# Kernel tuning notes

Measured on AMD Instinct MI355X. Metric: run time of the kernel, lower is better.

## Reference

```python
import jax, jax.numpy as jnp
import numpy as np

M, B, N, C, H = 3, 8, 512, 512, 8
HD = C // H
W_SCALE = 0.02  # keep attention logits in a sane range


def setup_inputs() -> dict:
    key = jax.random.key(0)
    ks = jax.random.split(key, 10)
    f32 = jnp.float32
    return {
        "x": jax.random.normal(ks[0], (M, B, N, C), f32),
        "Wq": jax.random.normal(ks[1], (M, C, C), f32) * W_SCALE,
        "bq": jax.random.normal(ks[2], (M, C), f32) * W_SCALE,
        "Wk": jax.random.normal(ks[3], (M, C, C), f32) * W_SCALE,
        "bk": jax.random.normal(ks[4], (M, C), f32) * W_SCALE,
        "Wv": jax.random.normal(ks[5], (M, C, C), f32) * W_SCALE,
        "bv": jax.random.normal(ks[6], (M, C), f32) * W_SCALE,
        "mw": jnp.ones((M, M), f32),
        "Wp": jax.random.normal(ks[7], (C, C), f32) * W_SCALE,
        "bp": jax.random.normal(ks[8], (C,), f32) * W_SCALE,
    }


def reference(x, Wq, bq, Wk, bk, Wv, bv, mw, Wp, bp):
    # x: [M,B,N,C] stacked modality features
    m, b, n, c = x.shape
    h, hd = H, c // H
    scale = hd ** -0.5

    def project(W, bias):
        y = jnp.einsum('mbnc,mcd->mbnd', x, W) + bias[:, None, None, :]
        return y.reshape(m, b, n, h, hd).transpose(0, 1, 3, 2, 4)  # [M,B,H,N,hd]

    q = project(Wq, bq)
    k = project(Wk, bk)
    v = project(Wv, bv)

    # all M*M pairwise attentions: i = query modality, j = key/value modality
    scores = jnp.einsum('ibhnd,jbhkd->ijbhnk', q, k) * scale  # [M,M,B,H,N,N]
    probs = jax.nn.softmax(scores, axis=-1)
    out = jnp.einsum('ijbhnk,jbhkd->ijbhnd', probs, v)
    out = out * mw[:, :, None, None, None, None]  # per-pair modal weight

    # sum over key-modality j, then mean over query-modality i
    fused = out.sum(axis=1).mean(axis=0)  # [B,H,N,hd]
    fused = fused.transpose(0, 2, 1, 3).reshape(b, n, c)  # [B,N,C]

    return jnp.einsum('bnc,cd->bnd', fused, Wp) + bp
```

## Files before the change

### kernel.cpp

```cpp
#include <hip/hip_runtime.h>
#include <stdint.h>

#define M_ 3
#define B_ 8
#define N_ 512
#define C_ 512
#define H_ 8
#define HD_ 64

typedef __bf16 bf16x8 __attribute__((ext_vector_type(8)));
typedef float f32x4 __attribute__((ext_vector_type(4)));
typedef float f32x16 __attribute__((ext_vector_type(16)));
typedef unsigned int u32x4 __attribute__((ext_vector_type(4)));

static __device__ __forceinline__ unsigned short f2bf(float f) {
  unsigned int u = __float_as_uint(f);
  unsigned int r = (u + 0x7FFFu + ((u >> 16) & 1u)) >> 16;
  return (unsigned short)r;
}
static __device__ __forceinline__ float bf2f(unsigned short s) {
  return __uint_as_float(((unsigned int)s) << 16);
}

static __device__ __forceinline__ void gll16(const void* g, void* l) {
  __builtin_amdgcn_global_load_lds(
      (const __attribute__((address_space(1))) unsigned int*)g,
      (__attribute__((address_space(3))) unsigned int*)l, 16, 0, 0);
}

__global__ void convert_x_kernel(const float* __restrict__ x,
                                 unsigned short* __restrict__ xb, int n4) {
  int i = blockIdx.x * 256 + threadIdx.x;
  if (i < n4) {
    float4 v = ((const float4*)x)[i];
    ushort4 o;
    o.x = f2bf(v.x); o.y = f2bf(v.y); o.z = f2bf(v.z); o.w = f2bf(v.w);
    ((ushort4*)xb)[i] = o;
  }
}

__global__ void transpose_w_kernel(const float* __restrict__ Wq, const float* __restrict__ Wk,
                                   const float* __restrict__ Wv, const float* __restrict__ Wp,
                                   unsigned short* __restrict__ Wqt, unsigned short* __restrict__ Wkt,
                                   unsigned short* __restrict__ Wvt, unsigned short* __restrict__ Wpt) {
  int z = blockIdx.z;
  const float* src; unsigned short* dst;
  if (z < 3)      { src = Wq + z * 262144;      dst = Wqt + z * 262144; }
  else if (z < 6) { src = Wk + (z - 3) * 262144; dst = Wkt + (z - 3) * 262144; }
  else if (z < 9) { src = Wv + (z - 6) * 262144; dst = Wvt + (z - 6) * 262144; }
  else            { src = Wp;                    dst = Wpt; }
  __shared__ unsigned short t[64][68];
  int r0 = blockIdx.x * 64, c0 = blockIdx.y * 64;
  int tr = threadIdx.x >> 4, tc = (threadIdx.x & 15) * 4;
#pragma unroll
  for (int it = 0; it < 4; ++it) {
    int r = tr + it * 16;
    float4 v = *(const float4*)&src[(size_t)(r0 + r) * 512 + c0 + tc];
    t[tc + 0][r] = f2bf(v.x); t[tc + 1][r] = f2bf(v.y);
    t[tc + 2][r] = f2bf(v.z); t[tc + 3][r] = f2bf(v.w);
  }
  __syncthreads();
#pragma unroll
  for (int it = 0; it < 4; ++it) {
    int d = tr + it * 16;
    ushort4 o;
    o.x = t[d][tc + 0]; o.y = t[d][tc + 1]; o.z = t[d][tc + 2]; o.w = t[d][tc + 3];
    *(ushort4*)&dst[(size_t)(c0 + d) * 512 + r0 + tc] = o;
  }
}

template <int MODE>
__launch_bounds__(256, 2)
__global__ void gemm128_kernel(const unsigned short* __restrict__ Aall,
                               const unsigned short* __restrict__ Bt0,
                               const unsigned short* __restrict__ Bt1,
                               const unsigned short* __restrict__ Bt2,
                               const float* __restrict__ bias0,
                               const float* __restrict__ bias1,
                               const float* __restrict__ bias2,
                               unsigned short* __restrict__ outQ,
                               unsigned short* __restrict__ outK,
                               unsigned short* __restrict__ outVt,
                               float* __restrict__ outF) {
  const int tid = threadIdx.x;
  const int wv = tid >> 6, l = tid & 63;
  const int wr = wv >> 1, wc = wv & 1;
  const int bm = blockIdx.x, bn = blockIdx.y;
  int m = 0, p = 0;
  const unsigned short* A; const unsigned short* Bt; const float* bias;
  if (MODE == 0) {
    int z = blockIdx.z; m = z / 3; p = z % 3;
    A = Aall + (size_t)m * (B_ * N_ * C_);
    Bt = (p == 0 ? Bt0 : p == 1 ? Bt1 : Bt2) + (size_t)m * (C_ * C_);
    bias = (p == 0 ? bias0 : p == 1 ? bias1 : bias2) + m * C_;
  } else {
    A = Aall; Bt = Bt0; bias = bias0;
  }
  __shared__ __align__(16) unsigned short lA[2][128 * 64];
  __shared__ __align__(16) unsigned short lB[2][128 * 64];
  f32x4 acc[4][4] = {};

  auto stage = [&](int buf, int kt) {
    int k0 = kt * 64;
#pragma unroll
    for (int it = 0; it < 4; ++it) {
      int f = (it * 256 + tid) * 16;
      int r = f >> 7, o = f & 127;
      int so = o ^ ((r & 7) << 4);
      gll16((const char*)A + ((size_t)(bm * 128 + r) * 512 + k0) * 2 + so,
            (char*)&lA[buf][0] + (it * 256 + wv * 64) * 16);
      gll16((const char*)Bt + ((size_t)(bn * 128 + r) * 512 + k0) * 2 + so,
            (char*)&lB[buf][0] + (it * 256 + wv * 64) * 16);
    }
  };

  stage(0, 0);
  __syncthreads();
  int buf = 0;
  for (int kt = 0; kt < 8; ++kt) {
    if (kt < 7) stage(buf ^ 1, kt + 1);
    bf16x8 aF[4][2], bF[4][2];
#pragma unroll
    for (int rt = 0; rt < 4; ++rt)
#pragma unroll
      for (int kf = 0; kf < 2; ++kf) {
        int rowA = wr * 64 + rt * 16 + (l & 15);
        int rowB = wc * 64 + rt * 16 + (l & 15);
        int kb = kf * 64 + (l >> 4) * 16;
        aF[rt][kf] = *(const bf16x8*)((const char*)&lA[buf][0] + rowA * 128 + (kb ^ ((rowA & 7) << 4)));
        bF[rt][kf] = *(const bf16x8*)((const char*)&lB[buf][0] + rowB * 128 + (kb ^ ((rowB & 7) << 4)));
      }
#pragma unroll
    for (int kf = 0; kf < 2; ++kf)
#pragma unroll
      for (int rt = 0; rt < 4; ++rt)
#pragma unroll
        for (int ct = 0; ct < 4; ++ct)
          acc[rt][ct] = __builtin_amdgcn_mfma_f32_16x16x32_bf16(aF[rt][kf], bF[ct][kf], acc[rt][ct], 0, 0, 0);
    __syncthreads();
    buf ^= 1;
  }

#pragma unroll
  for (int rt = 0; rt < 4; ++rt) {
    int rbase = bm * 128 + wr * 64 + rt * 16 + (l >> 4) * 4;
#pragma unroll
    for (int ct = 0; ct < 4; ++ct) {
      int col = bn * 128 + wc * 64 + ct * 16 + (l & 15);
      float bb = bias[col];
      if (MODE == 0) {
        int h = col >> 6, hd = col & 63;
        if (p < 2) {
          unsigned short* out = (p == 0 ? outQ : outK) + (size_t)m * (B_ * H_ * N_ * HD_);
#pragma unroll
          for (int jr = 0; jr < 4; ++jr) {
            int row = rbase + jr; int b = row >> 9, n = row & 511;
            out[(((size_t)(b * H_ + h) * N_ + n) * HD_) + hd] = f2bf(acc[rt][ct][jr] + bb);
          }
        } else {
          unsigned short* out = outVt + (size_t)m * (B_ * H_ * HD_ * N_);
          int row = rbase; int b = row >> 9, n = row & 511;
          ushort4 o;
          o.x = f2bf(acc[rt][ct][0] + bb);
          o.y = f2bf(acc[rt][ct][1] + bb);
          o.z = f2bf(acc[rt][ct][2] + bb);
          o.w = f2bf(acc[rt][ct][3] + bb);
          *(ushort4*)&out[(((size_t)(b * H_ + h) * HD_ + hd) * N_) + n] = o;
        }
      } else {
#pragma unroll
        for (int jr = 0; jr < 4; ++jr) {
          int row = rbase + jr;
          outF[(size_t)row * C_ + col] = acc[rt][ct][jr] + bb;
        }
      }
    }
  }
}

__launch_bounds__(256, 3)
__global__ void attn_kernel(const unsigned short* __restrict__ qg,
                            const unsigned short* __restrict__ kg,
                            const unsigned short* __restrict__ vg,
                            const float* __restrict__ mw,
                            unsigned short* __restrict__ att) {
  const int tid = threadIdx.x;
  const int wv = tid >> 6, l = tid & 63;
  const int hi = l >> 5, lq = l & 31;
  const int xcd = blockIdx.x & 7, slot = blockIdx.x >> 3;
  const int bh = (xcd << 3) | (slot & 7);
  const int qi = slot >> 3;
  const int qt = qi & 3, i = qi >> 2;
  const int b = bh >> 3, h = bh & 7;
  const int n0 = qt * 128;

  __shared__ __align__(16) unsigned short lK[2][64 * 64];
  __shared__ __align__(16) unsigned short lV[2][64 * 64];

  bf16x8 qB[4];
  {
    const unsigned short* qb = qg + (size_t)((i * B_ + b) * H_ + h) * N_ * HD_;
    int n = n0 + wv * 32 + lq;
#pragma unroll
    for (int ks = 0; ks < 4; ++ks)
      qB[ks] = *(const bf16x8*)&qb[(size_t)n * HD_ + ks * 16 + hi * 8];
  }

  f32x16 facc[2] = {};
  const float scale = 0.125f;

  for (int j = 0; j < 3; ++j) {
    const char* kb = (const char*)(kg + (size_t)((j * B_ + b) * H_ + h) * N_ * HD_);
    const char* vb = (const char*)(vg + (size_t)((j * B_ + b) * H_ + h) * HD_ * N_);
    auto stage = [&](int buf, int kt) {
#pragma unroll
      for (int it = 0; it < 2; ++it) {
        int f = (it * 256 + tid) * 16;
        int r = f >> 7, o = f & 127;
        int so = o ^ ((r & 7) << 4);
        gll16(kb + kt * 8192 + (f & ~127) + so, (char*)&lK[buf][0] + (it * 256 + wv * 64) * 16);
        gll16(vb + r * 1024 + kt * 128 + so,    (char*)&lV[buf][0] + (it * 256 + wv * 64) * 16);
      }
    };
    stage(0, 0);
    __syncthreads();
    f32x16 oacc[2] = {};
    float dAcc = 0.0f;
    int buf = 0;
    for (int kt = 0; kt < 8; ++kt) {
      if (kt < 7) stage(buf ^ 1, kt + 1);
#pragma unroll
      for (int kt2 = 0; kt2 < 2; ++kt2) {
        f32x16 sT = {};
#pragma unroll
        for (int ks = 0; ks < 4; ++ks) {
          int row = kt2 * 32 + lq;
          int col = (ks * 32 + hi * 16) ^ ((row & 7) << 4);
          bf16x8 kA = *(const bf16x8*)((const char*)&lK[buf][0] + row * 128 + col);
          sT = __builtin_amdgcn_mfma_f32_32x32x16_bf16(kA, qB[ks], sT, 0, 0, 0);
        }
        unsigned int c[8];
#pragma unroll
        for (int w = 0; w < 8; ++w) {
          float pa = __expf(sT[2 * w] * scale);
          float pb = __expf(sT[2 * w + 1] * scale);
          dAcc += pa + pb;
          c[w] = (unsigned int)f2bf(pa) | ((unsigned int)f2bf(pb) << 16);
        }
#pragma unroll
        for (int hs = 0; hs < 2; ++hs) {
          int ks = kt2 * 2 + hs;
          unsigned int p0 = (unsigned int)__shfl_xor((int)c[4 * hs + 0], 32, 64);
          unsigned int p1 = (unsigned int)__shfl_xor((int)c[4 * hs + 1], 32, 64);
          unsigned int p2 = (unsigned int)__shfl_xor((int)c[4 * hs + 2], 32, 64);
          unsigned int p3 = (unsigned int)__shfl_xor((int)c[4 * hs + 3], 32, 64);
          u32x4 pw;
          pw.x = hi ? p2 : c[4 * hs + 0];
          pw.y = hi ? p3 : c[4 * hs + 1];
          pw.z = hi ? c[4 * hs + 2] : p0;
          pw.w = hi ? c[4 * hs + 3] : p1;
          bf16x8 pA = __builtin_bit_cast(bf16x8, pw);
#pragma unroll
          for (int ht = 0; ht < 2; ++ht) {
            int row = ht * 32 + lq;
            int col = (ks * 32 + hi * 16) ^ ((row & 7) << 4);
            bf16x8 vB = *(const bf16x8*)((const char*)&lV[buf][0] + row * 128 + col);
            oacc[ht] = __builtin_amdgcn_mfma_f32_32x32x16_bf16(pA, vB, oacc[ht], 0, 0, 0);
          }
        }
      }
      __syncthreads();
      buf ^= 1;
    }
    float den = dAcc + __shfl_xor(dAcc, 32, 64);
    float t = mw[i * 3 + j] * (1.0f / 3.0f) / den;
#pragma unroll
    for (int reg = 0; reg < 16; ++reg) {
      int kkq = (reg & 3) + 8 * (reg >> 2) + 4 * hi;
      float tr = __shfl(t, kkq, 64);
      facc[0][reg] += oacc[0][reg] * tr;
      facc[1][reg] += oacc[1][reg] * tr;
    }
  }
  unsigned short* outp = att + (size_t)i * (B_ * N_ * C_);
#pragma unroll
  for (int ht = 0; ht < 2; ++ht)
#pragma unroll
    for (int reg = 0; reg < 16; ++reg) {
      int n = n0 + wv * 32 + (reg & 3) + 8 * (reg >> 2) + 4 * hi;
      int cc = h * 64 + ht * 32 + lq;
      outp[((size_t)b * N_ + n) * C_ + cc] = f2bf(facc[ht][reg]);
    }
}

__global__ void sum3_kernel(const unsigned short* __restrict__ a0,
                            const unsigned short* __restrict__ a1,
                            const unsigned short* __restrict__ a2,
                            unsigned short* __restrict__ o, int n4) {
  int idx = blockIdx.x * 256 + threadIdx.x;
  if (idx < n4) {
    ushort4 x0 = ((const ushort4*)a0)[idx];
    ushort4 x1 = ((const ushort4*)a1)[idx];
    ushort4 x2 = ((const ushort4*)a2)[idx];
    ushort4 r;
    r.x = f2bf(bf2f(x0.x) + bf2f(x1.x) + bf2f(x2.x));
    r.y = f2bf(bf2f(x0.y) + bf2f(x1.y) + bf2f(x2.y));
    r.z = f2bf(bf2f(x0.z) + bf2f(x1.z) + bf2f(x2.z));
    r.w = f2bf(bf2f(x0.w) + bf2f(x1.w) + bf2f(x2.w));
    ((ushort4*)o)[idx] = r;
  }
}

extern "C" void kernel_launch(void* const* d_in, const int* in_sizes, int n_in,
                              void* d_out, int out_size, void* d_ws, size_t ws_size,
                              hipStream_t stream) {
  const float* x  = (const float*)d_in[0];
  const float* Wq = (const float*)d_in[1];
  const float* bq = (const float*)d_in[2];
  const float* Wk = (const float*)d_in[3];
  const float* bk = (const float*)d_in[4];
  const float* Wv = (const float*)d_in[5];
  const float* bv = (const float*)d_in[6];
  const float* mw = (const float*)d_in[7];
  const float* Wp = (const float*)d_in[8];
  const float* bp = (const float*)d_in[9];
  float* out = (float*)d_out;

  char* ws = (char*)d_ws;
  size_t off = 0;
  auto alloc = [&](size_t elems) {
    unsigned short* pp = (unsigned short*)(ws + off);
    off += elems * 2; off = (off + 255) & ~(size_t)255;
    return pp;
  };
  unsigned short* xb  = alloc((size_t)M_ * B_ * N_ * C_);
  unsigned short* Wqt = alloc((size_t)M_ * C_ * C_);
  unsigned short* Wkt = alloc((size_t)M_ * C_ * C_);
  unsigned short* Wvt = alloc((size_t)M_ * C_ * C_);
  unsigned short* Wpt = alloc((size_t)C_ * C_);
  unsigned short* qb  = alloc((size_t)M_ * B_ * H_ * N_ * HD_);
  unsigned short* kb  = alloc((size_t)M_ * B_ * H_ * N_ * HD_);
  unsigned short* vtb = alloc((size_t)M_ * B_ * H_ * HD_ * N_);
  unsigned short* att = alloc((size_t)M_ * B_ * N_ * C_);
  unsigned short* fb  = alloc((size_t)B_ * N_ * C_);

  convert_x_kernel<<<6144, 256, 0, stream>>>(x, xb, (M_ * B_ * N_ * C_) / 4);
  transpose_w_kernel<<<dim3(8, 8, 10), 256, 0, stream>>>(Wq, Wk, Wv, Wp, Wqt, Wkt, Wvt, Wpt);
  gemm128_kernel<0><<<dim3(32, 4, 9), 256, 0, stream>>>(xb, Wqt, Wkt, Wvt, bq, bk, bv,
                                                        qb, kb, vtb, nullptr);
  attn_kernel<<<768, 256, 0, stream>>>(qb, kb, vtb, mw, att);
  sum3_kernel<<<2048, 256, 0, stream>>>(att, att + (size_t)B_ * N_ * C_,
                                        att + (size_t)2 * B_ * N_ * C_, fb,
                                        (B_ * N_ * C_) / 4);
  gemm128_kernel<1><<<dim3(32, 4, 1), 256, 0, stream>>>(fb, Wpt, nullptr, nullptr, bp, nullptr, nullptr,
                                                        nullptr, nullptr, nullptr, out);
}
```

Measured before the change: 214.5 us.

## Split attention over all nine modality pairs, fold softmax scale into K

The attention grid grows from one block per query modality to one block per (query, key) modality pair, and each pair writes its own buffer. A new sum9 kernel reduces the nine buffers. Softmax scale and log2(e) are pre-multiplied into K in the projection GEMM so the kernel can use exp2 directly, and the row denominator is computed with an MFMA against a ones vector instead of scalar adds. Occupancy bounds are raised, which gives more parallelism and shorter serial chains per block, at the cost of extra global traffic for nine intermediate tensors. There is also a slight accuracy change because the denominator is summed from bf16-rounded probabilities.

Result: faster. 201.7 us (-6.0%).

```diff
diff --git a/kernel.cpp b/kernel.cpp
--- a/kernel.cpp
+++ b/kernel.cpp
@@ -9,9 +9,18 @@
 #define HD_ 64
 
 typedef __bf16 bf16x8 __attribute__((ext_vector_type(8)));
+typedef __bf16 bf16x2 __attribute__((ext_vector_type(2)));
 typedef float f32x4 __attribute__((ext_vector_type(4)));
 typedef float f32x16 __attribute__((ext_vector_type(16)));
 typedef unsigned int u32x4 __attribute__((ext_vector_type(4)));
+
+#if __has_builtin(__builtin_amdgcn_exp2f)
+#define EXP2(x) __builtin_amdgcn_exp2f(x)
+#else
+#define EXP2(x) __expf((x)*0.69314718056f)
+#endif
+
+#define K_PRESCALE 0.18033688f
 
 static __device__ __forceinline__ unsigned short f2bf(float f) {
   unsigned int u = __float_as_uint(f);
@@ -141,6 +150,7 @@
     buf ^= 1;
   }
 
+  const float vscale = (MODE == 0 && p == 1) ? K_PRESCALE : 1.0f;
 #pragma unroll
   for (int rt = 0; rt < 4; ++rt) {
     int rbase = bm * 128 + wr * 64 + rt * 16 + (l >> 4) * 4;
@@ -155,7 +165,7 @@
 #pragma unroll
           for (int jr = 0; jr < 4; ++jr) {
             int row = rbase + jr; int b = row >> 9, n = row & 511;
-            out[(((size_t)(b * H_ + h) * N_ + n) * HD_) + hd] = f2bf(acc[rt][ct][jr] + bb);
+            out[(((size_t)(b * H_ + h) * N_ + n) * HD_) + hd] = f2bf((acc[rt][ct][jr] + bb) * vscale);
           }
         } else {
           unsigned short* out = outVt + (size_t)m * (B_ * H_ * HD_ * N_);
@@ -178,19 +188,20 @@
   }
 }
 
-__launch_bounds__(256, 3)
+__launch_bounds__(256, 4)
 __global__ void attn_kernel(const unsigned short* __restrict__ qg,
                             const unsigned short* __restrict__ kg,
                             const unsigned short* __restrict__ vg,
                             const float* __restrict__ mw,
-                            unsigned short* __restrict__ att) {
+                            unsigned short* __restrict__ att9) {
   const int tid = threadIdx.x;
   const int wv = tid >> 6, l = tid & 63;
   const int hi = l >> 5, lq = l & 31;
   const int xcd = blockIdx.x & 7, slot = blockIdx.x >> 3;
   const int bh = (xcd << 3) | (slot & 7);
-  const int qi = slot >> 3;
-  const int qt = qi & 3, i = qi >> 2;
+  const int r_ = slot >> 3;
+  const int qt = r_ & 3, ij = r_ >> 2;
+  const int i = ij / 3, j = ij % 3;
   const int b = bh >> 3, h = bh & 7;
   const int n0 = qt * 128;
 
@@ -205,110 +216,112 @@
     for (int ks = 0; ks < 4; ++ks)
       qB[ks] = *(const bf16x8*)&qb[(size_t)n * HD_ + ks * 16 + hi * 8];
   }
-
-  f32x16 facc[2] = {};
-  const float scale = 0.125f;
-
-  for (int j = 0; j < 3; ++j) {
-    const char* kb = (const char*)(kg + (size_t)((j * B_ + b) * H_ + h) * N_ * HD_);
-    const char* vb = (const char*)(vg + (size_t)((j * B_ + b) * H_ + h) * HD_ * N_);
-    auto stage = [&](int buf, int kt) {
-#pragma unroll
-      for (int it = 0; it < 2; ++it) {
-        int f = (it * 256 + tid) * 16;
-        int r = f >> 7, o = f & 127;
-        int so = o ^ ((r & 7) << 4);
-        gll16(kb + kt * 8192 + (f & ~127) + so, (char*)&lK[buf][0] + (it * 256 + wv * 64) * 16);
-        gll16(vb + r * 1024 + kt * 128 + so,    (char*)&lV[buf][0] + (it * 256 + wv * 64) * 16);
-      }
-    };
-    stage(0, 0);
+  bf16x8 onesB;
+#pragma unroll
+  for (int zz = 0; zz < 8; ++zz) onesB[zz] = (__bf16)1.0f;
+
+  const char* kb = (const char*)(kg + (size_t)((j * B_ + b) * H_ + h) * N_ * HD_);
+  const char* vb = (const char*)(vg + (size_t)((j * B_ + b) * H_ + h) * HD_ * N_);
+  auto stage = [&](int buf, int kt) {
+#pragma unroll
+    for (int it = 0; it < 2; ++it) {
+      int f = (it * 256 + tid) * 16;
+      int r = f >> 7, o = f & 127;
+      int so = o ^ ((r & 7) << 4);
+      gll16(kb + kt * 8192 + (f & ~127) + so, (char*)&lK[buf][0] + (it * 256 + wv * 64) * 16);
+      gll16(vb + r * 1024 + kt * 128 + so,    (char*)&lV[buf][0] + (it * 256 + wv * 64) * 16);
+    }
+  };
+  stage(0, 0);
+  __syncthreads();
+
+  f32x16 oacc[2] = {};
+  f32x16 dacc = {};
+  int buf = 0;
+  for (int kt = 0; kt < 8; ++kt) {
+    if (kt < 7) stage(buf ^ 1, kt + 1);
+#pragma unroll
+    for (int kt2 = 0; kt2 < 2; ++kt2) {
+      f32x16 sT = {};
+#pragma unroll
+      for (int ks = 0; ks < 4; ++ks) {
+        int row = kt2 * 32 + lq;
+        int col = (ks * 32 + hi * 16) ^ ((row & 7) << 4);
+        bf16x8 kA = *(const bf16x8*)((const char*)&lK[buf][0] + row * 128 + col);
+        sT = __builtin_amdgcn_mfma_f32_32x32x16_bf16(kA, qB[ks], sT, 0, 0, 0);
+      }
+      unsigned int c[8];
+#pragma unroll
+      for (int w = 0; w < 8; ++w) {
+        bf16x2 t2;
+        t2[0] = (__bf16)EXP2(sT[2 * w]);
+        t2[1] = (__bf16)EXP2(sT[2 * w + 1]);
+        c[w] = __builtin_bit_cast(unsigned int, t2);
+      }
+#pragma unroll
+      for (int hs = 0; hs < 2; ++hs) {
+        int ks = kt2 * 2 + hs;
+        unsigned int s0 = hi ? c[4 * hs + 0] : c[4 * hs + 2];
+        unsigned int s1 = hi ? c[4 * hs + 1] : c[4 * hs + 3];
+        unsigned int r0 = (unsigned int)__shfl_xor((int)s0, 32, 64);
+        unsigned int r1 = (unsigned int)__shfl_xor((int)s1, 32, 64);
+        u32x4 pw;
+        pw.x = hi ? r0 : c[4 * hs + 0];
+        pw.y = hi ? r1 : c[4 * hs + 1];
+        pw.z = hi ? c[4 * hs + 2] : r0;
+        pw.w = hi ? c[4 * hs + 3] : r1;
+        bf16x8 pA = __builtin_bit_cast(bf16x8, pw);
+        dacc = __builtin_amdgcn_mfma_f32_32x32x16_bf16(pA, onesB, dacc, 0, 0, 0);
+#pragma unroll
+        for (int ht = 0; ht < 2; ++ht) {
+          int row = ht * 32 + lq;
+          int col = (ks * 32 + hi * 16) ^ ((row & 7) << 4);
+          bf16x8 vB = *(const bf16x8*)((const char*)&lV[buf][0] + row * 128 + col);
+          oacc[ht] = __builtin_amdgcn_mfma_f32_32x32x16_bf16(pA, vB, oacc[ht], 0, 0, 0);
+        }
+      }
+    }
     __syncthreads();
-    f32x16 oacc[2] = {};
-    float dAcc = 0.0f;
-    int buf = 0;
-    for (int kt = 0; kt < 8; ++kt) {
-      if (kt < 7) stage(buf ^ 1, kt + 1);
-#pragma unroll
-      for (int kt2 = 0; kt2 < 2; ++kt2) {
-        f32x16 sT = {};
-#pragma unroll
-        for (int ks = 0; ks < 4; ++ks) {
-          int row = kt2 * 32 + lq;
-          int col = (ks * 32 + hi * 16) ^ ((row & 7) << 4);
-          bf16x8 kA = *(const bf16x8*)((const char*)&lK[buf][0] + row * 128 + col);
-          sT = __builtin_amdgcn_mfma_f32_32x32x16_bf16(kA, qB[ks], sT, 0, 0, 0);
-        }
-        unsigned int c[8];
-#pragma unroll
-        for (int w = 0; w < 8; ++w) {
-          float pa = __expf(sT[2 * w] * scale);
-          float pb = __expf(sT[2 * w + 1] * scale);
-          dAcc += pa + pb;
-          c[w] = (unsigned int)f2bf(pa) | ((unsigned int)f2bf(pb) << 16);
-        }
-#pragma unroll
-        for (int hs = 0; hs < 2; ++hs) {
-          int ks = kt2 * 2 + hs;
-          unsigned int p0 = (unsigned int)__shfl_xor((int)c[4 * hs + 0], 32, 64);
-          unsigned int p1 = (unsigned int)__shfl_xor((int)c[4 * hs + 1], 32, 64);
-          unsigned int p2 = (unsigned int)__shfl_xor((int)c[4 * hs + 2], 32, 64);
-          unsigned int p3 = (unsigned int)__shfl_xor((int)c[4 * hs + 3], 32, 64);
-          u32x4 pw;
-          pw.x = hi ? p2 : c[4 * hs + 0];
-          pw.y = hi ? p3 : c[4 * hs + 1];
-          pw.z = hi ? c[4 * hs + 2] : p0;
-          pw.w = hi ? c[4 * hs + 3] : p1;
-          bf16x8 pA = __builtin_bit_cast(bf16x8, pw);
-#pragma unroll
-          for (int ht = 0; ht < 2; ++ht) {
-            int row = ht * 32 + lq;
-            int col = (ks * 32 + hi * 16) ^ ((row & 7) << 4);
-            bf16x8 vB = *(const bf16x8*)((const char*)&lV[buf][0] + row * 128 + col);
-            oacc[ht] = __builtin_amdgcn_mfma_f32_32x32x16_bf16(pA, vB, oacc[ht], 0, 0, 0);
-          }
-        }
-      }
-      __syncthreads();
-      buf ^= 1;
-    }
-    float den = dAcc + __shfl_xor(dAcc, 32, 64);
-    float t = mw[i * 3 + j] * (1.0f / 3.0f) / den;
-#pragma unroll
-    for (int reg = 0; reg < 16; ++reg) {
-      int kkq = (reg & 3) + 8 * (reg >> 2) + 4 * hi;
-      float tr = __shfl(t, kkq, 64);
-      facc[0][reg] += oacc[0][reg] * tr;
-      facc[1][reg] += oacc[1][reg] * tr;
-    }
-  }
-  unsigned short* outp = att + (size_t)i * (B_ * N_ * C_);
-#pragma unroll
-  for (int ht = 0; ht < 2; ++ht)
-#pragma unroll
-    for (int reg = 0; reg < 16; ++reg) {
-      int n = n0 + wv * 32 + (reg & 3) + 8 * (reg >> 2) + 4 * hi;
+    buf ^= 1;
+  }
+
+  float w = mw[ij] * (1.0f / 3.0f);
+  unsigned short* outp = att9 + (size_t)ij * (B_ * N_ * C_);
+#pragma unroll
+  for (int reg = 0; reg < 16; ++reg) {
+    float t = w / dacc[reg];
+    int n = n0 + wv * 32 + (reg & 3) + 8 * (reg >> 2) + 4 * hi;
+#pragma unroll
+    for (int ht = 0; ht < 2; ++ht) {
       int cc = h * 64 + ht * 32 + lq;
-      outp[((size_t)b * N_ + n) * C_ + cc] = f2bf(facc[ht][reg]);
-    }
-}
-
-__global__ void sum3_kernel(const unsigned short* __restrict__ a0,
-                            const unsigned short* __restrict__ a1,
-                            const unsigned short* __restrict__ a2,
-                            unsigned short* __restrict__ o, int n4) {
+      outp[((size_t)b * N_ + n) * C_ + cc] = f2bf(oacc[ht][reg] * t);
+    }
+  }
+}
+
+__global__ void sum9_kernel(const unsigned short* __restrict__ att9,
+                            unsigned short* __restrict__ o, int n8) {
   int idx = blockIdx.x * 256 + threadIdx.x;
-  if (idx < n4) {
-    ushort4 x0 = ((const ushort4*)a0)[idx];
-    ushort4 x1 = ((const ushort4*)a1)[idx];
-    ushort4 x2 = ((const ushort4*)a2)[idx];
-    ushort4 r;
-    r.x = f2bf(bf2f(x0.x) + bf2f(x1.x) + bf2f(x2.x));
-    r.y = f2bf(bf2f(x0.y) + bf2f(x1.y) + bf2f(x2.y));
-    r.z = f2bf(bf2f(x0.z) + bf2f(x1.z) + bf2f(x2.z));
-    r.w = f2bf(bf2f(x0.w) + bf2f(x1.w) + bf2f(x2.w));
-    ((ushort4*)o)[idx] = r;
-  }
+  if (idx >= n8) return;
+  float acc[8] = {};
+#pragma unroll
+  for (int s = 0; s < 9; ++s) {
+    uint4 v = ((const uint4*)(att9 + (size_t)s * (B_ * N_ * C_)))[idx];
+    acc[0] += bf2f((unsigned short)(v.x & 0xffff));
+    acc[1] += bf2f((unsigned short)(v.x >> 16));
+    acc[2] += bf2f((unsigned short)(v.y & 0xffff));
+    acc[3] += bf2f((unsigned short)(v.y >> 16));
+    acc[4] += bf2f((unsigned short)(v.z & 0xffff));
+    acc[5] += bf2f((unsigned short)(v.z >> 16));
+    acc[6] += bf2f((unsigned short)(v.w & 0xffff));
+    acc[7] += bf2f((unsigned short)(v.w >> 16));
+  }
+  uint4 r;
+  r.x = (unsigned int)f2bf(acc[0]) | ((unsigned int)f2bf(acc[1]) << 16);
+  r.y = (unsigned int)f2bf(acc[2]) | ((unsigned int)f2bf(acc[3]) << 16);
+  r.z = (unsigned int)f2bf(acc[4]) | ((unsigned int)f2bf(acc[5]) << 16);
+  r.w = (unsigned int)f2bf(acc[6]) | ((unsigned int)f2bf(acc[7]) << 16);
+  ((uint4*)o)[idx] = r;
 }
 
 extern "C" void kernel_launch(void* const* d_in, const int* in_sizes, int n_in,
@@ -333,25 +346,23 @@
     off += elems * 2; off = (off + 255) & ~(size_t)255;
     return pp;
   };
-  unsigned short* xb  = alloc((size_t)M_ * B_ * N_ * C_);
-  unsigned short* Wqt = alloc((size_t)M_ * C_ * C_);
-  unsigned short* Wkt = alloc((size_t)M_ * C_ * C_);
-  unsigned short* Wvt = alloc((size_t)M_ * C_ * C_);
-  unsigned short* Wpt = alloc((size_t)C_ * C_);
-  unsigned short* qb  = alloc((size_t)M_ * B_ * H_ * N_ * HD_);
-  unsigned short* kb  = alloc((size_t)M_ * B_ * H_ * N_ * HD_);
-  unsigned short* vtb = alloc((size_t)M_ * B_ * H_ * HD_ * N_);
-  unsigned short* att = alloc((size_t)M_ * B_ * N_ * C_);
-  unsigned short* fb  = alloc((size_t)B_ * N_ * C_);
+  unsigned short* xb   = alloc((size_t)M_ * B_ * N_ * C_);
+  unsigned short* Wqt  = alloc((size_t)M_ * C_ * C_);
+  unsigned short* Wkt  = alloc((size_t)M_ * C_ * C_);
+  unsigned short* Wvt  = alloc((size_t)M_ * C_ * C_);
+  unsigned short* Wpt  = alloc((size_t)C_ * C_);
+  unsigned short* qb   = alloc((size_t)M_ * B_ * H_ * N_ * HD_);
+  unsigned short* kb   = alloc((size_t)M_ * B_ * H_ * N_ * HD_);
+  unsigned short* vtb  = alloc((size_t)M_ * B_ * H_ * HD_ * N_);
+  unsigned short* att9 = alloc((size_t)9 * B_ * N_ * C_);
+  unsigned short* fb   = alloc((size_t)B_ * N_ * C_);
 
   convert_x_kernel<<<6144, 256, 0, stream>>>(x, xb, (M_ * B_ * N_ * C_) / 4);
   transpose_w_kernel<<<dim3(8, 8, 10), 256, 0, stream>>>(Wq, Wk, Wv, Wp, Wqt, Wkt, Wvt, Wpt);
   gemm128_kernel<0><<<dim3(32, 4, 9), 256, 0, stream>>>(xb, Wqt, Wkt, Wvt, bq, bk, bv,
                                                         qb, kb, vtb, nullptr);
-  attn_kernel<<<768, 256, 0, stream>>>(qb, kb, vtb, mw, att);
-  sum3_kernel<<<2048, 256, 0, stream>>>(att, att + (size_t)B_ * N_ * C_,
-                                        att + (size_t)2 * B_ * N_ * C_, fb,
-                                        (B_ * N_ * C_) / 4);
+  attn_kernel<<<2304, 256, 0, stream>>>(qb, kb, vtb, mw, att9);
+  sum9_kernel<<<1024, 256, 0, stream>>>(att9, fb, (B_ * N_ * C_) / 8);
   gemm128_kernel<1><<<dim3(32, 4, 1), 256, 0, stream>>>(fb, Wpt, nullptr, nullptr, bp, nullptr, nullptr,
                                                         nullptr, nullptr, nullptr, out);
 }
```
